# Performance work log

Measured on AMD Instinct MI355X. Metric: run time of the kernel, lower is better.

## Reference

```python
import jax, jax.numpy as jnp
import numpy as np

DIM = 1024
HEADS = 16
HEAD_DIM = DIM // HEADS
HIDDEN = 4096  # mlp_ratio * dim
SCALE = HEAD_DIM ** -0.5
LN_EPS = 1e-5


def softmax_one(x):
    # softmax with +1 in the denominator (after max subtraction), per source
    m = jnp.max(x, axis=-1, keepdims=True)
    e = jnp.exp(x - m)
    return e / (1.0 + jnp.sum(e, axis=-1, keepdims=True))


def layer_norm(x, g, b):
    mu = jnp.mean(x, axis=-1, keepdims=True)
    var = jnp.mean(jnp.square(x - mu), axis=-1, keepdims=True)
    return (x - mu) * jax.lax.rsqrt(var + LN_EPS) * g + b


def setup_inputs() -> dict:
    key = jax.random.key(0)
    ks = jax.random.split(key, 12)
    B, C, N = 2, DIM, 2048
    x = jax.random.normal(ks[0], (B, C, N), dtype=jnp.float32)
    mask = jax.random.randint(ks[1], (B, HEADS, N), 0, 2, dtype=jnp.int32)
    s = 0.02
    return {
        'x': x,
        'mask': mask,
        'qkv_w': jax.random.normal(ks[2], (3 * DIM, DIM), jnp.float32) * s,
        'qkv_b': jnp.zeros((3 * DIM,), jnp.float32),
        'proj_w': jax.random.normal(ks[3], (DIM, DIM), jnp.float32) * s,
        'proj_b': jnp.zeros((DIM,), jnp.float32),
        'fc1_w': jax.random.normal(ks[4], (HIDDEN, DIM), jnp.float32) * s,
        'fc1_b': jnp.zeros((HIDDEN,), jnp.float32),
        'ln_g': jnp.ones((HIDDEN,), jnp.float32),
        'ln_b': jnp.zeros((HIDDEN,), jnp.float32),
        'fc2_w': jax.random.normal(ks[5], (DIM, HIDDEN), jnp.float32) * s,
        'fc2_b': jnp.zeros((DIM,), jnp.float32),
    }


def reference(x, mask, qkv_w, qkv_b, proj_w, proj_b, fc1_w, fc1_b, ln_g, ln_b, fc2_w, fc2_b):
    B, C, N = x.shape
    xt = jnp.swapaxes(x, 1, 2)  # (B, N, C)

    # ----- attention -----
    qkv = xt @ qkv_w.T + qkv_b                      # (B, N, 3C)
    qkv = qkv.reshape(B, N, 3, HEADS, HEAD_DIM)
    qkv = jnp.transpose(qkv, (2, 0, 3, 1, 4))       # (3, B, H, N, Dh)
    q, k, v = qkv[0], qkv[1], qkv[2]
    scores = jnp.einsum('bhnd,bhmd->bhnm', q * SCALE, k)  # (B, H, N, N)
    scores = jnp.where(mask[:, :, :, None] == 0, -1e9, scores)
    attn = softmax_one(scores)
    out = jnp.einsum('bhnm,bhmd->bhnd', attn, v)    # (B, H, N, Dh)
    # faithful to source: permute(0,3,1,2).reshape(B,N,C) -> scrambled merge
    out = jnp.transpose(out, (0, 3, 1, 2)).reshape(B, N, C)
    out = out @ proj_w.T + proj_b

    # faithful residual: attn_out + ls1(attn_out) with ls1 = Identity
    h = out + out                                   # (B, N, C)

    # ----- MLP (timm Mlp: fc1 -> GELU -> LayerNorm -> fc2) -----
    m = h @ fc1_w.T + fc1_b
    m = jax.nn.gelu(m, approximate=False)
    m = layer_norm(m, ln_g, ln_b)
    m = m @ fc2_w.T + fc2_b
    y = h + m                                       # (B, N, C)

    return jnp.swapaxes(y, 1, 2)                    # (B, C, N)
```

## Files before the change

### kernel.cpp

```cpp
#include <hip/hip_runtime.h>
#include <math.h>

#define DIMC   1024
#define NTOK   2048
#define BATCH  2
#define HEADS  16
#define HDIM   64
#define HIDDEN 4096
#define MROWS  (BATCH*NTOK)
#define QSZ    ((size_t)BATCH*HEADS*NTOK*HDIM)
#define QSC    0.18033688f

typedef unsigned short ushort_t;
typedef __attribute__((ext_vector_type(8))) short short8;
typedef __attribute__((ext_vector_type(4))) float f32x4;
typedef __attribute__((ext_vector_type(4))) unsigned short us4;

__device__ __forceinline__ ushort_t f2b(float f) {
  union { float f; unsigned int u; } cv; cv.f = f;
  unsigned int u = cv.u;
  unsigned int r = (u + 0x7fffu + ((u >> 16) & 1u)) >> 16;
  return (ushort_t)r;
}

__device__ __forceinline__ float b2f(ushort_t b) {
  union { unsigned int u; float f; } cv; cv.u = ((unsigned int)b) << 16;
  return cv.f;
}

__device__ __forceinline__ float fexp2(float x) {
#if __has_builtin(__builtin_amdgcn_exp2f)
  return __builtin_amdgcn_exp2f(x);
#else
  return exp2f(x);
#endif
}

__device__ __forceinline__ void gl_lds16(const void* g, void* l) {
  __builtin_amdgcn_global_load_lds(
      (const __attribute__((address_space(1))) void*)g,
      (__attribute__((address_space(3))) void*)l, 16, 0, 0);
}

__device__ __forceinline__ void lds_barrier() {
  __builtin_amdgcn_s_waitcnt(0xC07F);
  __builtin_amdgcn_s_barrier();
}

__global__ __launch_bounds__(256) void k_transpose(const float* __restrict__ x,
                                                   ushort_t* __restrict__ xt) {
  __shared__ float t[32][33];
  int b  = blockIdx.z;
  int c0 = blockIdx.y * 32, n0 = blockIdx.x * 32;
  int tx = threadIdx.x, ty = threadIdx.y;
#pragma unroll
  for (int l = 0; l < 4; l++)
    t[ty + l * 8][tx] = x[((size_t)(b * DIMC + c0 + ty + l * 8)) * NTOK + n0 + tx];
  __syncthreads();
#pragma unroll
  for (int l = 0; l < 4; l++)
    xt[((size_t)(b * NTOK + n0 + ty + l * 8)) * DIMC + c0 + tx] = f2b(t[tx][ty + l * 8]);
}

__global__ __launch_bounds__(256) void k_f2b4(const float* __restrict__ w0,
                                              const float* __restrict__ w1,
                                              const float* __restrict__ w2,
                                              const float* __restrict__ w3,
                                              ushort_t* __restrict__ o0,
                                              ushort_t* __restrict__ o1,
                                              ushort_t* __restrict__ o2,
                                              ushort_t* __restrict__ o3) {
  int bid = blockIdx.x;
  const float* in; ushort_t* out; int base;
  if (bid < 3072)      { in = w0; out = o0; base = bid; }
  else if (bid < 4096) { in = w1; out = o1; base = bid - 3072; }
  else if (bid < 8192) { in = w2; out = o2; base = bid - 4096; }
  else                 { in = w3; out = o3; base = bid - 8192; }
  int i = base * 256 + threadIdx.x;
  float4 v = ((const float4*)in)[i];
  us4 o; o.x = f2b(v.x); o.y = f2b(v.y); o.z = f2b(v.z); o.w = f2b(v.w);
  ((us4*)out)[i] = o;
}

template <int EPI, int NTX8, int KDIM>
__global__ __launch_bounds__(256) void k_gemm_bf16(const ushort_t* __restrict__ A,
                                                   const ushort_t* __restrict__ W,
                                                   const float* __restrict__ bias,
                                                   void* __restrict__ outv,
                                                   const ushort_t* __restrict__ extra) {
  __shared__ ushort_t As[2][128 * 32];
  __shared__ ushort_t Bs[2][128 * 32];
  const int tid = threadIdx.x;
  const int lane = tid & 63, wv = tid >> 6;
  const int bid = blockIdx.x;
  const int xcd = bid & 7, t = bid >> 3;
  const int row0 = (t / NTX8) * 128;
  const int col0 = (xcd * NTX8 + (t % NTX8)) * 128;
  const int wrow0 = (wv >> 1) * 64, wcol0 = (wv & 1) * 64;
  const int lm = lane & 15, lq = lane >> 4;
  const int srow = wv * 32 + (lane >> 2);
  const int gch = (lane & 3) ^ ((lane >> 3) & 3);
  const int sslot = (lane & 3) * 8;
  const int sw8 = (lq ^ ((lm >> 1) & 3)) * 8;

  const ushort_t* Ab = A + (size_t)(row0 + srow) * KDIM + gch * 8;
  const ushort_t* Wb = W + (size_t)(col0 + srow) * KDIM + gch * 8;
  const size_t rstep = (size_t)16 * KDIM;

  short8 ga0[2], gb0[2], ga1[2], gb1[2];

  f32x4 acc[4][4];
#pragma unroll
  for (int i = 0; i < 4; i++)
#pragma unroll
    for (int j = 0; j < 4; j++) acc[i][j] = (f32x4){0.f, 0.f, 0.f, 0.f};

#define GLOAD(sl, k0) do {                                     \
    ga##sl[0] = *(const short8*)(Ab + (k0));                   \
    ga##sl[1] = *(const short8*)(Ab + rstep + (k0));           \
    gb##sl[0] = *(const short8*)(Wb + (k0));                   \
    gb##sl[1] = *(const short8*)(Wb + rstep + (k0));           \
  } while (0)
#define SWRITE(buf, sl) do {                                   \
    *(short8*)&As[buf][srow * 32 + sslot]        = ga##sl[0];  \
    *(short8*)&As[buf][(srow + 16) * 32 + sslot] = ga##sl[1];  \
    *(short8*)&Bs[buf][srow * 32 + sslot]        = gb##sl[0];  \
    *(short8*)&Bs[buf][(srow + 16) * 32 + sslot] = gb##sl[1];  \
  } while (0)

  auto compute = [&](int buf) {
    short8 af[4], bf[4];
#pragma unroll
    for (int mi = 0; mi < 4; mi++)
      af[mi] = *(const short8*)&As[buf][(wrow0 + mi * 16 + lm) * 32 + sw8];
#pragma unroll
    for (int ni = 0; ni < 4; ni++)
      bf[ni] = *(const short8*)&Bs[buf][(wcol0 + ni * 16 + lm) * 32 + sw8];
#pragma unroll
    for (int mi = 0; mi < 4; mi++)
#pragma unroll
      for (int ni = 0; ni < 4; ni++)
        acc[mi][ni] = __builtin_amdgcn_mfma_f32_16x16x32_bf16(af[mi], bf[ni], acc[mi][ni], 0, 0, 0);
  };

  constexpr int S = KDIM / 32;
  GLOAD(0, 0);
  GLOAD(1, 32);
  SWRITE(0, 0);

#pragma unroll 1
  for (int kk = 0; kk < S; kk += 2) {
    lds_barrier();
    if (kk + 2 < S) GLOAD(0, (kk + 2) * 32);
    SWRITE(1, 1);
    compute(0);
    lds_barrier();
    if (kk + 3 < S) GLOAD(1, (kk + 3) * 32);
    if (kk + 2 < S) SWRITE(0, 0);
    compute(1);
  }
#undef GLOAD
#undef SWRITE

#pragma unroll
  for (int mi = 0; mi < 4; mi++) {
#pragma unroll
    for (int ni = 0; ni < 4; ni++) {
#pragma unroll
      for (int r = 0; r < 4; r++) {
        const int row = row0 + wrow0 + mi * 16 + lq * 4 + r;
        const int col = col0 + wcol0 + ni * 16 + lm;
        float v = acc[mi][ni][r] + bias[col];
        if (EPI == 0) {
          int which = col >> 10, rem = col & 1023, hh = rem >> 6, d = rem & 63;
          int bb = row >> 11, n = row & 2047;
          size_t bh = (size_t)(bb * HEADS + hh);
          ushort_t* o16 = (ushort_t*)outv;
          if (which == 0)
            o16[(bh * NTOK + n) * HDIM + d] = f2b(v * QSC);
          else if (which == 1)
            o16[QSZ + (bh * NTOK + n) * HDIM + d] = f2b(v);
          else
            o16[2 * QSZ + (bh * HDIM + d) * NTOK + n] = f2b(v);
        } else if (EPI == 1) {
          ((ushort_t*)outv)[(size_t)row * DIMC + col] = f2b(2.f * v);
        } else if (EPI == 2) {
          ((ushort_t*)outv)[(size_t)row * HIDDEN + col] = f2b(v);
        } else {
          float y = b2f(extra[(size_t)row * DIMC + col]) + v;
          int bb = row >> 11, n = row & 2047;
          ((float*)outv)[((size_t)(bb * DIMC + col)) * NTOK + n] = y;
        }
      }
    }
  }
}

__global__ __launch_bounds__(256) void k_attn_mfma(const ushort_t* __restrict__ qkv,
                                                   const int* __restrict__ mask,
                                                   ushort_t* __restrict__ scram) {
  __shared__ ushort_t Kl[2][64 * 64];
  __shared__ ushort_t Vl[2][64 * 64];
  __shared__ ushort_t Pl[4 * 32 * 72];
  const int tid = threadIdx.x;
  const int lane = tid & 63, w = tid >> 6;
  const int lm = lane & 15, quad = lane >> 4;
  const int bh = blockIdx.y, b = bh >> 4, h = bh & 15;
  const int q0 = blockIdx.x * 128 + w * 32;
  const ushort_t* qg  = qkv + (size_t)bh * NTOK * HDIM;
  const ushort_t* kg  = qkv + QSZ + (size_t)bh * NTOK * HDIM;
  const ushort_t* vTg = qkv + 2 * QSZ + (size_t)bh * HDIM * NTOK;
  ushort_t* Pw = &Pl[w * 32 * 72];

  const short8 ones = {0x3F80, 0x3F80, 0x3F80, 0x3F80, 0x3F80, 0x3F80, 0x3F80, 0x3F80};

  short8 qf[2][2];
#pragma unroll
  for (int qs = 0; qs < 2; qs++)
#pragma unroll
    for (int hf = 0; hf < 2; hf++)
      qf[qs][hf] = *(const short8*)&qg[(size_t)(q0 + qs * 16 + lm) * HDIM + hf * 32 + quad * 8];

  bool mk[2][4];
#pragma unroll
  for (int qs = 0; qs < 2; qs++)
#pragma unroll
    for (int r = 0; r < 4; r++)
      mk[qs][r] = mask[(size_t)bh * NTOK + q0 + qs * 16 + quad * 4 + r] != 0;

  f32x4 O[2][4], La[2];
#pragma unroll
  for (int qs = 0; qs < 2; qs++) {
    La[qs] = (f32x4){0.f, 0.f, 0.f, 0.f};
#pragma unroll
    for (int r = 0; r < 4; r++) O[qs][r] = (f32x4){0.f, 0.f, 0.f, 0.f};
  }

  const int s0 = tid, s1 = tid + 256;
  const int r0 = s0 >> 3, g0 = (s0 & 7) ^ (r0 & 7);
  const int r1 = s1 >> 3, g1 = (s1 & 7) ^ (r1 & 7);

  gl_lds16(kg + (size_t)r0 * HDIM + g0 * 8, &Kl[0][s0 * 8]);
  gl_lds16(kg + (size_t)r1 * HDIM + g1 * 8, &Kl[0][s1 * 8]);
  gl_lds16(vTg + (size_t)r0 * NTOK + g0 * 8, &Vl[0][s0 * 8]);
  gl_lds16(vTg + (size_t)r1 * NTOK + g1 * 8, &Vl[0][s1 * 8]);

  for (int kt = 0; kt < NTOK; kt += 64) {
    const int cur = (kt >> 6) & 1, nxt = cur ^ 1;
    __syncthreads();
    if (kt + 64 < NTOK) {
      gl_lds16(kg + (size_t)(kt + 64 + r0) * HDIM + g0 * 8, &Kl[nxt][s0 * 8]);
      gl_lds16(kg + (size_t)(kt + 64 + r1) * HDIM + g1 * 8, &Kl[nxt][s1 * 8]);
      gl_lds16(vTg + (size_t)r0 * NTOK + kt + 64 + g0 * 8, &Vl[nxt][s0 * 8]);
      gl_lds16(vTg + (size_t)r1 * NTOK + kt + 64 + g1 * 8, &Vl[nxt][s1 * 8]);
    }

    short8 kf[4][2];
#pragma unroll
    for (int ksub = 0; ksub < 4; ksub++)
#pragma unroll
      for (int hf = 0; hf < 2; hf++)
        kf[ksub][hf] = *(const short8*)&Kl[cur][(ksub * 16 + lm) * 64 + ((4 * hf + quad) ^ (lm & 7)) * 8];

#pragma unroll
    for (int qs = 0; qs < 2; qs++) {
      f32x4 S[4];
#pragma unroll
      for (int ksub = 0; ksub < 4; ksub++) {
        S[ksub] = (f32x4){0.f, 0.f, 0.f, 0.f};
        S[ksub] = __builtin_amdgcn_mfma_f32_16x16x32_bf16(qf[qs][0], kf[ksub][0], S[ksub], 0, 0, 0);
        S[ksub] = __builtin_amdgcn_mfma_f32_16x16x32_bf16(qf[qs][1], kf[ksub][1], S[ksub], 0, 0, 0);
      }
#pragma unroll
      for (int r = 0; r < 4; r++) {
        const int prow = qs * 16 + quad * 4 + r;
#pragma unroll
        for (int ksub = 0; ksub < 4; ksub++) {
          float p = mk[qs][r] ? fexp2(S[ksub][r]) : 1.0f;
          Pw[prow * 72 + ksub * 16 + lm] = (ushort_t)(__float_as_uint(p) >> 16);
        }
      }
    }
    __builtin_amdgcn_s_waitcnt(0xC07F);

    short8 vf[4][2];
#pragma unroll
    for (int dsub = 0; dsub < 4; dsub++)
#pragma unroll
      for (int hf = 0; hf < 2; hf++)
        vf[dsub][hf] = *(const short8*)&Vl[cur][(dsub * 16 + lm) * 64 + ((4 * hf + quad) ^ (lm & 7)) * 8];

#pragma unroll
    for (int qs = 0; qs < 2; qs++) {
      short8 pf[2];
#pragma unroll
      for (int hf = 0; hf < 2; hf++)
        pf[hf] = *(const short8*)&Pw[(qs * 16 + lm) * 72 + hf * 32 + quad * 8];
#pragma unroll
      for (int dsub = 0; dsub < 4; dsub++) {
        O[qs][dsub] = __builtin_amdgcn_mfma_f32_16x16x32_bf16(pf[0], vf[dsub][0], O[qs][dsub], 0, 0, 0);
        O[qs][dsub] = __builtin_amdgcn_mfma_f32_16x16x32_bf16(pf[1], vf[dsub][1], O[qs][dsub], 0, 0, 0);
      }
      La[qs] = __builtin_amdgcn_mfma_f32_16x16x32_bf16(pf[0], ones, La[qs], 0, 0, 0);
      La[qs] = __builtin_amdgcn_mfma_f32_16x16x32_bf16(pf[1], ones, La[qs], 0, 0, 0);
    }
  }

#pragma unroll
  for (int qs = 0; qs < 2; qs++)
#pragma unroll
    for (int r = 0; r < 4; r++) {
      int n = q0 + qs * 16 + quad * 4 + r;
      float inv = 1.f / (1.f + La[qs][r]);
      int n1 = n >> 10, nn0 = n & 1023;
#pragma unroll
      for (int dsub = 0; dsub < 4; dsub++) {
        int d = dsub * 16 + lm;
        int np = d * 32 + h * 2 + n1;
        scram[((size_t)(b * NTOK + np)) * DIMC + nn0] = f2b(O[qs][dsub][r] * inv);
      }
    }
}

__global__ __launch_bounds__(256) void k_ln(ushort_t* __restrict__ mid,
                                            const float* __restrict__ g,
                                            const float* __restrict__ bta) {
  const int row = blockIdx.x;
  ushort_t* p = mid + (size_t)row * HIDDEN;
  const int tid = threadIdx.x;
  float lv[16];
  float s = 0.f, s2 = 0.f;
#pragma unroll
  for (int i = 0; i < 4; i++) {
    us4 u = *(const us4*)&p[tid * 4 + i * 1024];
#pragma unroll
    for (int j = 0; j < 4; j++) {
      float xx = b2f((j == 0) ? u.x : (j == 1) ? u.y : (j == 2) ? u.z : u.w);
      xx = 0.5f * xx * (1.f + erff(xx * 0.70710678118654752f));
      lv[i * 4 + j] = xx;
      s += xx;
      s2 += xx * xx;
    }
  }
#pragma unroll
  for (int off = 32; off > 0; off >>= 1) {
    s += __shfl_down(s, off);
    s2 += __shfl_down(s2, off);
  }
  __shared__ float rs[4], rs2[4];
  if ((tid & 63) == 0) { rs[tid >> 6] = s; rs2[tid >> 6] = s2; }
  __syncthreads();
  float ts = rs[0] + rs[1] + rs[2] + rs[3];
  float ts2 = rs2[0] + rs2[1] + rs2[2] + rs2[3];
  float mu = ts * (1.f / HIDDEN);
  float var = ts2 * (1.f / HIDDEN) - mu * mu;
  float rstd = rsqrtf(var + 1e-5f);
#pragma unroll
  for (int i = 0; i < 4; i++) {
    us4 o;
#pragma unroll
    for (int j = 0; j < 4; j++) {
      int f = tid * 4 + i * 1024 + j;
      float y = (lv[i * 4 + j] - mu) * rstd * g[f] + bta[f];
      ushort_t ob = f2b(y);
      if (j == 0) o.x = ob; else if (j == 1) o.y = ob; else if (j == 2) o.z = ob; else o.w = ob;
    }
    *(us4*)&p[tid * 4 + i * 1024] = o;
  }
}

extern "C" void kernel_launch(void* const* d_in, const int* in_sizes, int n_in,
                              void* d_out, int out_size, void* d_ws, size_t ws_size,
                              hipStream_t stream) {
  const float* x      = (const float*)d_in[0];
  const int*   mask   = (const int*)d_in[1];
  const float* qkv_w  = (const float*)d_in[2];
  const float* qkv_b  = (const float*)d_in[3];
  const float* proj_w = (const float*)d_in[4];
  const float* proj_b = (const float*)d_in[5];
  const float* fc1_w  = (const float*)d_in[6];
  const float* fc1_b  = (const float*)d_in[7];
  const float* ln_g   = (const float*)d_in[8];
  const float* ln_b   = (const float*)d_in[9];
  const float* fc2_w  = (const float*)d_in[10];
  const float* fc2_b  = (const float*)d_in[11];

  char* w = (char*)d_ws;
  ushort_t* qkv16  = (ushort_t*)w;           w += 3 * QSZ * 2;
  ushort_t* xtb    = (ushort_t*)w;           w += (size_t)MROWS * DIMC * 2;
  ushort_t* scramb = (ushort_t*)w;           w += (size_t)MROWS * DIMC * 2;
  ushort_t* hb     = (ushort_t*)w;           w += (size_t)MROWS * DIMC * 2;
  ushort_t* mid    = (ushort_t*)w;           w += (size_t)MROWS * HIDDEN * 2;
  ushort_t* wqkvb  = (ushort_t*)w;           w += (size_t)3 * DIMC * DIMC * 2;
  ushort_t* wprojb = (ushort_t*)w;           w += (size_t)DIMC * DIMC * 2;
  ushort_t* wfc1b  = (ushort_t*)w;           w += (size_t)HIDDEN * DIMC * 2;
  ushort_t* wfc2b  = (ushort_t*)w;           w += (size_t)DIMC * HIDDEN * 2;

  k_transpose<<<dim3(NTOK / 32, DIMC / 32, BATCH), dim3(32, 8), 0, stream>>>(x, xtb);
  k_f2b4<<<dim3(12288), 256, 0, stream>>>(qkv_w, proj_w, fc1_w, fc2_w,
                                          wqkvb, wprojb, wfc1b, wfc2b);

  k_gemm_bf16<0, 3, DIMC><<<dim3(24 * 32), 256, 0, stream>>>(
      xtb, wqkvb, qkv_b, qkv16, nullptr);
  k_attn_mfma<<<dim3(NTOK / 128, BATCH * HEADS), 256, 0, stream>>>(
      qkv16, mask, scramb);
  k_gemm_bf16<1, 1, DIMC><<<dim3(8 * 32), 256, 0, stream>>>(
      scramb, wprojb, proj_b, hb, nullptr);
  k_gemm_bf16<2, 4, DIMC><<<dim3(32 * 32), 256, 0, stream>>>(
      hb, wfc1b, fc1_b, mid, nullptr);
  k_ln<<<dim3(MROWS), 256, 0, stream>>>(mid, ln_g, ln_b);
  k_gemm_bf16<3, 1, HIDDEN><<<dim3(8 * 32), 256, 0, stream>>>(
      mid, wfc2b, fc2_b, d_out, hb);
}
```

Before: 391.8 us.

## Split-K the proj and fc2 GEMMs with separate combine kernels

The proj and fc2 GEMMs, which launch only 256 tiles on a GPU with 256 CUs, now run as 2-way split-K over a second grid dimension. Each half writes fp32 partials to a new workspace buffer. Small combine kernels then add the bias, the doubling or residual, and the output transpose. This aims to fix under-occupancy of those GEMMs, at the cost of writing and re-reading two fp32 partial buffers plus two extra kernel launches.

```diff
diff --git a/kernel.cpp b/kernel.cpp
--- a/kernel.cpp
+++ b/kernel.cpp
@@ -82,17 +82,16 @@
   ((us4*)out)[i] = o;
 }
 
-template <int EPI, int NTX8, int KDIM>
+template <int EPI, int NTX8, int KSTRIDE, int KLEN>
 __global__ __launch_bounds__(256) void k_gemm_bf16(const ushort_t* __restrict__ A,
                                                    const ushort_t* __restrict__ W,
                                                    const float* __restrict__ bias,
-                                                   void* __restrict__ outv,
-                                                   const ushort_t* __restrict__ extra) {
+                                                   void* __restrict__ outv) {
   __shared__ ushort_t As[2][128 * 32];
   __shared__ ushort_t Bs[2][128 * 32];
   const int tid = threadIdx.x;
   const int lane = tid & 63, wv = tid >> 6;
-  const int bid = blockIdx.x;
+  const int bid = blockIdx.x, kz = blockIdx.y;
   const int xcd = bid & 7, t = bid >> 3;
   const int row0 = (t / NTX8) * 128;
   const int col0 = (xcd * NTX8 + (t % NTX8)) * 128;
@@ -103,9 +102,9 @@
   const int sslot = (lane & 3) * 8;
   const int sw8 = (lq ^ ((lm >> 1) & 3)) * 8;
 
-  const ushort_t* Ab = A + (size_t)(row0 + srow) * KDIM + gch * 8;
-  const ushort_t* Wb = W + (size_t)(col0 + srow) * KDIM + gch * 8;
-  const size_t rstep = (size_t)16 * KDIM;
+  const ushort_t* Ab = A + (size_t)(row0 + srow) * KSTRIDE + (size_t)kz * KLEN + gch * 8;
+  const ushort_t* Wb = W + (size_t)(col0 + srow) * KSTRIDE + (size_t)kz * KLEN + gch * 8;
+  const size_t rstep = (size_t)16 * KSTRIDE;
 
   short8 ga0[2], gb0[2], ga1[2], gb1[2];
 
@@ -143,7 +142,7 @@
         acc[mi][ni] = __builtin_amdgcn_mfma_f32_16x16x32_bf16(af[mi], bf[ni], acc[mi][ni], 0, 0, 0);
   };
 
-  constexpr int S = KDIM / 32;
+  constexpr int S = KLEN / 32;
   GLOAD(0, 0);
   GLOAD(1, 32);
   SWRITE(0, 0);
@@ -170,7 +169,8 @@
       for (int r = 0; r < 4; r++) {
         const int row = row0 + wrow0 + mi * 16 + lq * 4 + r;
         const int col = col0 + wcol0 + ni * 16 + lm;
-        float v = acc[mi][ni][r] + bias[col];
+        float v = acc[mi][ni][r];
+        if (EPI != 4) v += bias[col];
         if (EPI == 0) {
           int which = col >> 10, rem = col & 1023, hh = rem >> 6, d = rem & 63;
           int bb = row >> 11, n = row & 2047;
@@ -182,18 +182,50 @@
             o16[QSZ + (bh * NTOK + n) * HDIM + d] = f2b(v);
           else
             o16[2 * QSZ + (bh * HDIM + d) * NTOK + n] = f2b(v);
-        } else if (EPI == 1) {
-          ((ushort_t*)outv)[(size_t)row * DIMC + col] = f2b(2.f * v);
         } else if (EPI == 2) {
           ((ushort_t*)outv)[(size_t)row * HIDDEN + col] = f2b(v);
         } else {
-          float y = b2f(extra[(size_t)row * DIMC + col]) + v;
-          int bb = row >> 11, n = row & 2047;
-          ((float*)outv)[((size_t)(bb * DIMC + col)) * NTOK + n] = y;
+          ((float*)outv)[(size_t)kz * MROWS * DIMC + (size_t)row * DIMC + col] = v;
         }
       }
     }
   }
+}
+
+__global__ __launch_bounds__(256) void k_comb_proj(const float* __restrict__ p0,
+                                                   const float* __restrict__ p1,
+                                                   const float* __restrict__ bias,
+                                                   ushort_t* __restrict__ hb) {
+  int i = blockIdx.x * 256 + threadIdx.x;
+  int colb = (i & 255) * 4;
+  float4 a = ((const float4*)p0)[i];
+  float4 b = ((const float4*)p1)[i];
+  us4 o;
+  o.x = f2b(2.f * (a.x + b.x + bias[colb + 0]));
+  o.y = f2b(2.f * (a.y + b.y + bias[colb + 1]));
+  o.z = f2b(2.f * (a.z + b.z + bias[colb + 2]));
+  o.w = f2b(2.f * (a.w + b.w + bias[colb + 3]));
+  ((us4*)hb)[i] = o;
+}
+
+__global__ __launch_bounds__(256) void k_comb_fc2(const float* __restrict__ p0,
+                                                  const float* __restrict__ p1,
+                                                  const ushort_t* __restrict__ hb,
+                                                  const float* __restrict__ bias,
+                                                  float* __restrict__ out) {
+  __shared__ float t[32][33];
+  int b  = blockIdx.z;
+  int c0 = blockIdx.y * 32, n0 = blockIdx.x * 32;
+  int tx = threadIdx.x, ty = threadIdx.y;
+#pragma unroll
+  for (int l = 0; l < 4; l++) {
+    size_t idx = ((size_t)(b * NTOK + n0 + ty + l * 8)) * DIMC + c0 + tx;
+    t[ty + l * 8][tx] = p0[idx] + p1[idx] + b2f(hb[idx]) + bias[c0 + tx];
+  }
+  __syncthreads();
+#pragma unroll
+  for (int l = 0; l < 4; l++)
+    out[((size_t)(b * DIMC + c0 + ty + l * 8)) * NTOK + n0 + tx] = t[tx][ty + l * 8];
 }
 
 __global__ __launch_bounds__(256) void k_attn_mfma(const ushort_t* __restrict__ qkv,
@@ -395,20 +427,25 @@
   ushort_t* wprojb = (ushort_t*)w;           w += (size_t)DIMC * DIMC * 2;
   ushort_t* wfc1b  = (ushort_t*)w;           w += (size_t)HIDDEN * DIMC * 2;
   ushort_t* wfc2b  = (ushort_t*)w;           w += (size_t)DIMC * HIDDEN * 2;
+  float*    pbuf   = (float*)w;              w += (size_t)2 * MROWS * DIMC * 4;
+  float*    pbuf1  = pbuf + (size_t)MROWS * DIMC;
 
   k_transpose<<<dim3(NTOK / 32, DIMC / 32, BATCH), dim3(32, 8), 0, stream>>>(x, xtb);
   k_f2b4<<<dim3(12288), 256, 0, stream>>>(qkv_w, proj_w, fc1_w, fc2_w,
                                           wqkvb, wprojb, wfc1b, wfc2b);
 
-  k_gemm_bf16<0, 3, DIMC><<<dim3(24 * 32), 256, 0, stream>>>(
-      xtb, wqkvb, qkv_b, qkv16, nullptr);
+  k_gemm_bf16<0, 3, DIMC, DIMC><<<dim3(24 * 32), 256, 0, stream>>>(
+      xtb, wqkvb, qkv_b, qkv16);
   k_attn_mfma<<<dim3(NTOK / 128, BATCH * HEADS), 256, 0, stream>>>(
       qkv16, mask, scramb);
-  k_gemm_bf16<1, 1, DIMC><<<dim3(8 * 32), 256, 0, stream>>>(
-      scramb, wprojb, proj_b, hb, nullptr);
-  k_gemm_bf16<2, 4, DIMC><<<dim3(32 * 32), 256, 0, stream>>>(
-      hb, wfc1b, fc1_b, mid, nullptr);
+  k_gemm_bf16<4, 1, DIMC, 512><<<dim3(8 * 32, 2), 256, 0, stream>>>(
+      scramb, wprojb, nullptr, pbuf);
+  k_comb_proj<<<dim3(4096), 256, 0, stream>>>(pbuf, pbuf1, proj_b, hb);
+  k_gemm_bf16<2, 4, DIMC, DIMC><<<dim3(32 * 32), 256, 0, stream>>>(
+      hb, wfc1b, fc1_b, mid);
   k_ln<<<dim3(MROWS), 256, 0, stream>>>(mid, ln_g, ln_b);
-  k_gemm_bf16<3, 1, HIDDEN><<<dim3(8 * 32), 256, 0, stream>>>(
-      mid, wfc2b, fc2_b, d_out, hb);
-}
+  k_gemm_bf16<4, 1, HIDDEN, 2048><<<dim3(8 * 32, 2), 256, 0, stream>>>(
+      mid, wfc2b, nullptr, pbuf);
+  k_comb_fc2<<<dim3(NTOK / 32, DIMC / 32, BATCH), dim3(32, 8), 0, stream>>>(
+      pbuf, pbuf1, hb, fc2_b, (float*)d_out);
+}
```

After: 389.7 us. No clear change (-0.6%).
